# Optimization experiments

Measured on AMD Instinct MI355X. Metric: run time of the kernel, lower is better.

Reference implementation:

```python
import jax, jax.numpy as jnp
import numpy as np

DIM = 768
NUM_HEADS = 12
HEAD_DIM = DIM // NUM_HEADS
ALL_HEAD_DIM = HEAD_DIM * NUM_HEADS
SCALE = HEAD_DIM ** -0.5


def setup_inputs() -> dict:
    key = jax.random.key(0)
    k1, k2, k3, k4 = jax.random.split(key, 4)
    B, N = 8, 1024
    x = jax.random.normal(k1, (B, N, DIM), dtype=jnp.float32)
    # qkv_bias=False -> no qkv bias; proj has bias (nn.Linear default)
    w_qkv = jax.random.normal(k2, (DIM, 3 * ALL_HEAD_DIM), dtype=jnp.float32) * (DIM ** -0.5)
    w_proj = jax.random.normal(k3, (ALL_HEAD_DIM, DIM), dtype=jnp.float32) * (ALL_HEAD_DIM ** -0.5)
    b_proj = jax.random.normal(k4, (DIM,), dtype=jnp.float32) * 0.02
    return {"x": x, "w_qkv": w_qkv, "w_proj": w_proj, "b_proj": b_proj}


def reference(x, w_qkv, w_proj, b_proj):
    B, N, C = x.shape
    qkv = (x @ w_qkv).reshape(B, N, 3, NUM_HEADS, HEAD_DIM)
    qkv = jnp.transpose(qkv, (2, 0, 3, 1, 4))  # [3, B, H, N, D]
    q, k, v = qkv[0], qkv[1], qkv[2]
    attn = jax.nn.softmax(jnp.einsum('bhnd,bhmd->bhnm', q * SCALE, k), axis=-1)
    out = jnp.einsum('bhnm,bhmd->bhnd', attn, v)  # [B, H, N, D]
    out = jnp.transpose(out, (0, 2, 1, 3)).reshape(B, N, ALL_HEAD_DIM)
    return out @ w_proj + b_proj
```

## Files before the change

kernel.cpp:

```cpp
#include <hip/hip_runtime.h>

#define NH 12
#define HD 64
#define SEQ 1024
#define BATCH 8
#define DIM 768
#define QKVN 2304
#define ROWS 8192

typedef __bf16 bf16x8 __attribute__((ext_vector_type(8)));
typedef float f32x4 __attribute__((ext_vector_type(4)));
typedef unsigned short u16x8 __attribute__((ext_vector_type(8)));
typedef unsigned short u16x4 __attribute__((ext_vector_type(4)));

__device__ __forceinline__ unsigned short f2bf(float f) {
  union { float f; unsigned int u; } c; c.f = f;
  unsigned int u = c.u;
  u += 0x7fffu + ((u >> 16) & 1u);
  return (unsigned short)(u >> 16);
}

__device__ __forceinline__ void gload_lds16(const unsigned short* g, unsigned short* l) {
  __builtin_amdgcn_global_load_lds(
      (const __attribute__((address_space(1))) void*)g,
      (__attribute__((address_space(3))) void*)l, 16, 0, 0);
}

__global__ void cvt_bf16(const float* __restrict__ src, unsigned short* __restrict__ dst, int n4) {
  int i = blockIdx.x * 256 + threadIdx.x;
  if (i >= n4) return;
  float4 v = ((const float4*)src)[i];
  u16x4 o;
  o.x = f2bf(v.x); o.y = f2bf(v.y); o.z = f2bf(v.z); o.w = f2bf(v.w);
  ((u16x4*)dst)[i] = o;
}

__global__ void transpose_bf16(const float* __restrict__ src, unsigned short* __restrict__ dst,
                               int R, int C) {
  __shared__ float tile[32][33];
  int tx = threadIdx.x & 31, ty = threadIdx.x >> 5;
  int c0 = blockIdx.x * 32, r0 = blockIdx.y * 32;
#pragma unroll
  for (int i = 0; i < 4; ++i)
    tile[ty + i * 8][tx] = src[(size_t)(r0 + ty + i * 8) * C + c0 + tx];
  __syncthreads();
#pragma unroll
  for (int i = 0; i < 4; ++i)
    dst[(size_t)(c0 + ty + i * 8) * R + r0 + tx] = f2bf(tile[tx][ty + i * 8]);
}

template <bool BF16_OUT, bool SCALE_Q>
__global__ __launch_bounds__(256, 3) void gemm128(
    const unsigned short* __restrict__ A, const unsigned short* __restrict__ BT,
    void* __restrict__ Cout, const float* __restrict__ bias, int M, int N, int K) {
  __shared__ unsigned short As[128 * 32];
  __shared__ unsigned short Bs[128 * 32];
  const int tid = threadIdx.x;
  const int wave = tid >> 6, lane = tid & 63, quad = lane >> 4, l16 = lane & 15;
  const int wm = wave >> 1, wn = wave & 1;
  const int bm = blockIdx.y * 128, bn = blockIdx.x * 128;

  f32x4 zero4 = {0.f, 0.f, 0.f, 0.f};
  f32x4 acc[4][4];
#pragma unroll
  for (int i = 0; i < 4; ++i)
#pragma unroll
    for (int j = 0; j < 4; ++j) acc[i][j] = zero4;

  const int nkt = K >> 5;
  for (int kt = 0; kt < nkt; ++kt) {
    __syncthreads();
    const int k0 = kt * 32;
#pragma unroll
    for (int i = 0; i < 2; ++i) {
      int c0 = wave * 64 + 256 * i;
      int c = c0 + lane;
      int r = c >> 2, kc = c & 3;
      gload_lds16(A + (size_t)(bm + r) * K + k0 + kc * 8, &As[c0 * 8]);
    }
#pragma unroll
    for (int i = 0; i < 2; ++i) {
      int c0 = wave * 64 + 256 * i;
      int c = c0 + lane;
      int r = c >> 2, kc = c & 3;
      gload_lds16(BT + (size_t)(bn + r) * K + k0 + kc * 8, &Bs[c0 * 8]);
    }
    __syncthreads();
    bf16x8 af[4], bf[4];
#pragma unroll
    for (int mt = 0; mt < 4; ++mt)
      af[mt] = *(const bf16x8*)&As[(wm * 64 + mt * 16 + l16) * 32 + quad * 8];
#pragma unroll
    for (int nt = 0; nt < 4; ++nt)
      bf[nt] = *(const bf16x8*)&Bs[(wn * 64 + nt * 16 + l16) * 32 + quad * 8];
#pragma unroll
    for (int mt = 0; mt < 4; ++mt)
#pragma unroll
      for (int nt = 0; nt < 4; ++nt)
        acc[mt][nt] = __builtin_amdgcn_mfma_f32_16x16x32_bf16(af[mt], bf[nt], acc[mt][nt], 0, 0, 0);
  }
#pragma unroll
  for (int mt = 0; mt < 4; ++mt)
#pragma unroll
    for (int nt = 0; nt < 4; ++nt) {
      int col = bn + wn * 64 + nt * 16 + l16;
      float bv = BF16_OUT ? 0.f : bias[col];
      float scl = (SCALE_Q && col < DIM) ? 0.125f : 1.0f;
#pragma unroll
      for (int r = 0; r < 4; ++r) {
        int row = bm + wm * 64 + mt * 16 + quad * 4 + r;
        float v = acc[mt][nt][r];
        if (BF16_OUT)
          ((unsigned short*)Cout)[(size_t)row * N + col] = f2bf(v * scl);
        else
          ((float*)Cout)[(size_t)row * N + col] = v + bv;
      }
    }
}

__global__ __launch_bounds__(256, 5) void attn_kernel(
    const unsigned short* __restrict__ qkv, unsigned short* __restrict__ out) {
  __shared__ unsigned short Ks[2 * 64 * 32];
  __shared__ unsigned short Vts[64 * 72];
  __shared__ unsigned short Ps[64 * 68];

  const int tid = threadIdx.x;
  const int wave = tid >> 6, lane = tid & 63, quad = lane >> 4, l16 = lane & 15;
  const int x = blockIdx.x;
  const int qt = (x >> 3) & 15;
  const int bh = (x >> 7) * 8 + (x & 7);
  const int b = bh / NH, h = bh % NH;
  const int qcol = h * HD, kcol = DIM + h * HD, vcol = 2 * DIM + h * HD;
  const int rowQ0 = b * SEQ + qt * 64;
  const int rowKV0 = b * SEQ;

  bf16x8 qf[2];
  {
    const unsigned short* qp = qkv + (size_t)(rowQ0 + wave * 16 + l16) * QKVN + qcol + quad * 8;
    qf[0] = *(const bf16x8*)qp;
    qf[1] = *(const bf16x8*)(qp + 32);
  }

  f32x4 zero4 = {0.f, 0.f, 0.f, 0.f};
  f32x4 o[4];
  float lsum[4] = {0.f, 0.f, 0.f, 0.f};
#pragma unroll
  for (int dt = 0; dt < 4; ++dt) o[dt] = zero4;

  for (int jt = 0; jt < 16; ++jt) {
    __syncthreads();
#pragma unroll
    for (int i = 0; i < 2; ++i) {
      int c0 = wave * 64 + 256 * i;
      int c = c0 + lane;
      int kk = c >> 8, rem = c & 255, n = rem >> 2, kc = rem & 3;
      gload_lds16(qkv + (size_t)(rowKV0 + jt * 64 + n) * QKVN + kcol + kk * 32 + kc * 8, &Ks[c0 * 8]);
    }
    {
      int n0 = (tid & 31) * 2, d0 = (tid >> 5) * 8;
      u16x8 va = *(const u16x8*)(qkv + (size_t)(rowKV0 + jt * 64 + n0) * QKVN + vcol + d0);
      u16x8 vb = *(const u16x8*)(qkv + (size_t)(rowKV0 + jt * 64 + n0 + 1) * QKVN + vcol + d0);
#pragma unroll
      for (int e = 0; e < 8; ++e) {
        unsigned int w2 = (unsigned int)va[e] | ((unsigned int)vb[e] << 16);
        *(unsigned int*)&Vts[(d0 + e) * 72 + n0] = w2;
      }
    }
    __syncthreads();

    f32x4 s[4];
#pragma unroll
    for (int nt = 0; nt < 4; ++nt) s[nt] = zero4;
#pragma unroll
    for (int kk = 0; kk < 2; ++kk)
#pragma unroll
      for (int nt = 0; nt < 4; ++nt) {
        bf16x8 kf = *(const bf16x8*)&Ks[kk * 2048 + (nt * 16 + l16) * 32 + quad * 8];
        s[nt] = __builtin_amdgcn_mfma_f32_16x16x32_bf16(qf[kk], kf, s[nt], 0, 0, 0);
      }

#pragma unroll
    for (int nt = 0; nt < 4; ++nt)
#pragma unroll
      for (int r = 0; r < 4; ++r) {
        float p = __expf(s[nt][r]);
        lsum[r] += p;
        Ps[(wave * 16 + quad * 4 + r) * 68 + nt * 16 + l16] = f2bf(p);
      }
    __syncthreads();

#pragma unroll
    for (int kk = 0; kk < 2; ++kk) {
      int pb = (wave * 16 + l16) * 68 + kk * 32 + quad * 8;
      union { bf16x8 v; u16x4 h[2]; } pu;
      pu.h[0] = *(const u16x4*)&Ps[pb];
      pu.h[1] = *(const u16x4*)&Ps[pb + 4];
#pragma unroll
      for (int dt = 0; dt < 4; ++dt) {
        bf16x8 vf = *(const bf16x8*)&Vts[(dt * 16 + l16) * 72 + kk * 32 + quad * 8];
        o[dt] = __builtin_amdgcn_mfma_f32_16x16x32_bf16(pu.v, vf, o[dt], 0, 0, 0);
      }
    }
  }

#pragma unroll
  for (int r = 0; r < 4; ++r) {
    float l = lsum[r];
    l += __shfl_xor(l, 1);
    l += __shfl_xor(l, 2);
    l += __shfl_xor(l, 4);
    l += __shfl_xor(l, 8);
    float inv = 1.f / l;
    int row = rowQ0 + wave * 16 + quad * 4 + r;
#pragma unroll
    for (int dt = 0; dt < 4; ++dt)
      out[(size_t)row * DIM + h * HD + dt * 16 + l16] = f2bf(o[dt][r] * inv);
  }
}

extern "C" void kernel_launch(void* const* d_in, const int* in_sizes, int n_in,
                              void* d_out, int out_size, void* d_ws, size_t ws_size,
                              hipStream_t stream) {
  const float* x = (const float*)d_in[0];
  const float* w_qkv = (const float*)d_in[1];
  const float* w_proj = (const float*)d_in[2];
  const float* b_proj = (const float*)d_in[3];
  float* outp = (float*)d_out;

  unsigned short* xb = (unsigned short*)d_ws;
  unsigned short* wqkvT = xb + (size_t)ROWS * DIM;
  unsigned short* wprojT = wqkvT + (size_t)QKVN * DIM;
  unsigned short* qkvb = wprojT + (size_t)DIM * DIM;
  unsigned short* attnb = xb;

  cvt_bf16<<<(ROWS * DIM / 4 + 255) / 256, 256, 0, stream>>>(x, xb, ROWS * DIM / 4);
  transpose_bf16<<<dim3(QKVN / 32, DIM / 32), 256, 0, stream>>>(w_qkv, wqkvT, DIM, QKVN);
  transpose_bf16<<<dim3(DIM / 32, DIM / 32), 256, 0, stream>>>(w_proj, wprojT, DIM, DIM);
  gemm128<true, true><<<dim3(QKVN / 128, ROWS / 128), 256, 0, stream>>>(xb, wqkvT, qkvb, nullptr, ROWS, QKVN, DIM);
  attn_kernel<<<dim3(16 * 96), 256, 0, stream>>>(qkvb, attnb);
  gemm128<false, false><<<dim3(DIM / 128, ROWS / 128), 256, 0, stream>>>(attnb, wprojT, outp, b_proj, ROWS, DIM, DIM);
}
```

Measured before the change: 211.1 us.

## Restructure attention: 128-row tiles, double-buffered K/V, register-resident P

The attention kernel now uses 512-thread blocks covering 128 query rows, so each K/V tile loaded into LDS serves twice as many queries. K and V tiles are double-buffered: the next tile's K is fetched via global_load_lds and V is prefetched into registers while the current tile computes, leaving one barrier per iteration instead of three. The QK^T MFMA operands are swapped so the score layout matches the A-operand layout of the 16x16x16 bf16 MFMA, which lets P stay in registers with no LDS round trip. The trade-off is more LDS per block and more registers, while the row sum is reduced across lanes with shuffles.

```diff
diff --git a/kernel.cpp b/kernel.cpp
--- a/kernel.cpp
+++ b/kernel.cpp
@@ -12,6 +12,7 @@
 typedef float f32x4 __attribute__((ext_vector_type(4)));
 typedef unsigned short u16x8 __attribute__((ext_vector_type(8)));
 typedef unsigned short u16x4 __attribute__((ext_vector_type(4)));
+typedef short s16x4 __attribute__((ext_vector_type(4)));
 
 __device__ __forceinline__ unsigned short f2bf(float f) {
   union { float f; unsigned int u; } c; c.f = f;
@@ -118,21 +119,27 @@
     }
 }
 
-__global__ __launch_bounds__(256, 5) void attn_kernel(
+#define VS 76
+__global__ __launch_bounds__(512, 6) void attn_kernel(
     const unsigned short* __restrict__ qkv, unsigned short* __restrict__ out) {
-  __shared__ unsigned short Ks[2 * 64 * 32];
-  __shared__ unsigned short Vts[64 * 72];
-  __shared__ unsigned short Ps[64 * 68];
+  __shared__ unsigned short Ks[2][64 * 64];
+  __shared__ unsigned short Vts[2][64 * VS];
 
   const int tid = threadIdx.x;
   const int wave = tid >> 6, lane = tid & 63, quad = lane >> 4, l16 = lane & 15;
   const int x = blockIdx.x;
-  const int qt = (x >> 3) & 15;
-  const int bh = (x >> 7) * 8 + (x & 7);
+  const int qt = (x >> 3) & 7;
+  const int bh = (x & 7) + 8 * (x >> 6);
   const int b = bh / NH, h = bh % NH;
   const int qcol = h * HD, kcol = DIM + h * HD, vcol = 2 * DIM + h * HD;
-  const int rowQ0 = b * SEQ + qt * 64;
+  const int rowQ0 = b * SEQ + qt * 128;
   const int rowKV0 = b * SEQ;
+
+  const int kk_s = tid >> 8, rem_s = tid & 255, n_s = rem_s >> 2, kc_s = rem_s & 3;
+  const unsigned short* kgp = qkv + (size_t)(rowKV0 + n_s) * QKVN + kcol + kk_s * 32 + kc_s * 8;
+  unsigned short* klp = &Ks[0][0] + (tid & ~63) * 8;
+  const int vn = tid & 63, vd0 = (tid >> 6) * 8;
+  const unsigned short* vgp = qkv + (size_t)(rowKV0 + vn) * QKVN + vcol + vd0;
 
   bf16x8 qf[2];
   {
@@ -141,32 +148,30 @@
     qf[1] = *(const bf16x8*)(qp + 32);
   }
 
+  u16x8 vreg = *(const u16x8*)vgp;
+  gload_lds16(kgp, klp);
+  {
+    unsigned short* vb = &Vts[0][0];
+#pragma unroll
+    for (int e = 0; e < 8; ++e)
+      vb[(vd0 + e) * VS + vn] = vreg[e];
+  }
+
   f32x4 zero4 = {0.f, 0.f, 0.f, 0.f};
   f32x4 o[4];
-  float lsum[4] = {0.f, 0.f, 0.f, 0.f};
 #pragma unroll
   for (int dt = 0; dt < 4; ++dt) o[dt] = zero4;
+  float lsum = 0.f;
 
   for (int jt = 0; jt < 16; ++jt) {
+    u16x8 vnext;
+    if (jt < 15) vnext = *(const u16x8*)(vgp + (size_t)(jt + 1) * 64 * QKVN);
     __syncthreads();
-#pragma unroll
-    for (int i = 0; i < 2; ++i) {
-      int c0 = wave * 64 + 256 * i;
-      int c = c0 + lane;
-      int kk = c >> 8, rem = c & 255, n = rem >> 2, kc = rem & 3;
-      gload_lds16(qkv + (size_t)(rowKV0 + jt * 64 + n) * QKVN + kcol + kk * 32 + kc * 8, &Ks[c0 * 8]);
-    }
-    {
-      int n0 = (tid & 31) * 2, d0 = (tid >> 5) * 8;
-      u16x8 va = *(const u16x8*)(qkv + (size_t)(rowKV0 + jt * 64 + n0) * QKVN + vcol + d0);
-      u16x8 vb = *(const u16x8*)(qkv + (size_t)(rowKV0 + jt * 64 + n0 + 1) * QKVN + vcol + d0);
-#pragma unroll
-      for (int e = 0; e < 8; ++e) {
-        unsigned int w2 = (unsigned int)va[e] | ((unsigned int)vb[e] << 16);
-        *(unsigned int*)&Vts[(d0 + e) * 72 + n0] = w2;
-      }
-    }
-    __syncthreads();
+    if (jt < 15)
+      gload_lds16(kgp + (size_t)(jt + 1) * 64 * QKVN, klp + ((jt + 1) & 1) * 4096);
+
+    const unsigned short* Kb = &Ks[jt & 1][0];
+    const unsigned short* Vb = &Vts[jt & 1][0];
 
     f32x4 s[4];
 #pragma unroll
@@ -175,42 +180,42 @@
     for (int kk = 0; kk < 2; ++kk)
 #pragma unroll
       for (int nt = 0; nt < 4; ++nt) {
-        bf16x8 kf = *(const bf16x8*)&Ks[kk * 2048 + (nt * 16 + l16) * 32 + quad * 8];
-        s[nt] = __builtin_amdgcn_mfma_f32_16x16x32_bf16(qf[kk], kf, s[nt], 0, 0, 0);
-      }
-
+        bf16x8 kf = *(const bf16x8*)&Kb[kk * 2048 + (nt * 16 + l16) * 32 + quad * 8];
+        s[nt] = __builtin_amdgcn_mfma_f32_16x16x32_bf16(kf, qf[kk], s[nt], 0, 0, 0);
+      }
+
+    s16x4 pf[4];
 #pragma unroll
     for (int nt = 0; nt < 4; ++nt)
 #pragma unroll
       for (int r = 0; r < 4; ++r) {
         float p = __expf(s[nt][r]);
-        lsum[r] += p;
-        Ps[(wave * 16 + quad * 4 + r) * 68 + nt * 16 + l16] = f2bf(p);
-      }
-    __syncthreads();
-
-#pragma unroll
-    for (int kk = 0; kk < 2; ++kk) {
-      int pb = (wave * 16 + l16) * 68 + kk * 32 + quad * 8;
-      union { bf16x8 v; u16x4 h[2]; } pu;
-      pu.h[0] = *(const u16x4*)&Ps[pb];
-      pu.h[1] = *(const u16x4*)&Ps[pb + 4];
+        lsum += p;
+        pf[nt][r] = (short)f2bf(p);
+      }
+
+#pragma unroll
+    for (int nt = 0; nt < 4; ++nt)
 #pragma unroll
       for (int dt = 0; dt < 4; ++dt) {
-        bf16x8 vf = *(const bf16x8*)&Vts[(dt * 16 + l16) * 72 + kk * 32 + quad * 8];
-        o[dt] = __builtin_amdgcn_mfma_f32_16x16x32_bf16(pu.v, vf, o[dt], 0, 0, 0);
-      }
-    }
-  }
-
+        s16x4 vv = *(const s16x4*)&Vb[(dt * 16 + l16) * VS + nt * 16 + quad * 4];
+        o[dt] = __builtin_amdgcn_mfma_f32_16x16x16bf16_1k(pf[nt], vv, o[dt], 0, 0, 0);
+      }
+
+    if (jt < 15) {
+      unsigned short* vb = &Vts[(jt + 1) & 1][0];
+#pragma unroll
+      for (int e = 0; e < 8; ++e)
+        vb[(vd0 + e) * VS + vn] = vnext[e];
+    }
+  }
+
+  float l = lsum;
+  l += __shfl_xor(l, 16);
+  l += __shfl_xor(l, 32);
 #pragma unroll
   for (int r = 0; r < 4; ++r) {
-    float l = lsum[r];
-    l += __shfl_xor(l, 1);
-    l += __shfl_xor(l, 2);
-    l += __shfl_xor(l, 4);
-    l += __shfl_xor(l, 8);
-    float inv = 1.f / l;
+    float inv = 1.f / __shfl(l, quad * 4 + r);
     int row = rowQ0 + wave * 16 + quad * 4 + r;
 #pragma unroll
     for (int dt = 0; dt < 4; ++dt)
@@ -237,6 +242,6 @@
   transpose_bf16<<<dim3(QKVN / 32, DIM / 32), 256, 0, stream>>>(w_qkv, wqkvT, DIM, QKVN);
   transpose_bf16<<<dim3(DIM / 32, DIM / 32), 256, 0, stream>>>(w_proj, wprojT, DIM, DIM);
   gemm128<true, true><<<dim3(QKVN / 128, ROWS / 128), 256, 0, stream>>>(xb, wqkvT, qkvb, nullptr, ROWS, QKVN, DIM);
-  attn_kernel<<<dim3(16 * 96), 256, 0, stream>>>(qkvb, attnb);
+  attn_kernel<<<dim3(8 * 96), 512, 0, stream>>>(qkvb, attnb);
   gemm128<false, false><<<dim3(DIM / 128, ROWS / 128), 256, 0, stream>>>(attnb, wprojT, outp, b_proj, ROWS, DIM, DIM);
 }
```

New measurement: 199.7 us. 5.4% less time.
